# Kernel optimization log

Measured on AMD Instinct MI355X. Metric: run time of the kernel, lower is better.

Reference implementation:

```python
import jax, jax.numpy as jnp
import numpy as np

N, E, F, H, O, B = 100000, 1200000, 64, 1024, 1, 256


def _gcn_conv(x, W, b, src, dst, ew, num_nodes):
    # PyG GCNConv: out_i = sum_{(s->i)} d_i^{-1/2} w_e d_s^{-1/2} (x_s W) + b
    deg = jax.ops.segment_sum(ew, dst, num_segments=num_nodes)
    dinv = jnp.where(deg > 0, jax.lax.rsqrt(jnp.maximum(deg, 1e-12)), 0.0)
    norm = dinv[src] * ew * dinv[dst]          # [E]
    h = x @ W                                   # [N, out]
    msg = h[src] * norm[:, None]                # gather + scale
    return jax.ops.segment_sum(msg, dst, num_segments=num_nodes) + b


def setup_inputs() -> dict:
    key = jax.random.key(0)
    ks = jax.random.split(key, 12)
    def lin(k, fan_in, fan_out):
        s = 1.0 / np.sqrt(fan_in)
        kw, kb = jax.random.split(k)
        return (jax.random.uniform(kw, (fan_in, fan_out), jnp.float32, -s, s),
                jax.random.uniform(kb, (fan_out,), jnp.float32, -s, s))
    W1, b1 = lin(ks[0], F, F)
    W2, b2 = lin(ks[1], F, 2 * F)
    W3, b3 = lin(ks[2], 2 * F, 4 * F)
    Wf1, bf1 = lin(ks[3], 5 * F, H)
    Wf2, bf2 = lin(ks[4], H, O)
    feature = jax.random.normal(ks[5], (N, F), jnp.float32)
    edge_index = jax.random.randint(ks[6], (2, E), 0, N, jnp.int32)
    weight = jax.random.uniform(ks[7], (E,), jnp.float32)
    protein_batch = jnp.sort(jax.random.randint(ks[8], (N,), 0, B, jnp.int32))
    return {"feature": feature, "edge_index": edge_index, "weight": weight,
            "protein_batch": protein_batch,
            "W1": W1, "b1": b1, "W2": W2, "b2": b2, "W3": W3, "b3": b3,
            "Wf1": Wf1, "bf1": bf1, "Wf2": Wf2, "bf2": bf2}


def reference(feature, edge_index, weight, protein_batch,
              W1, b1, W2, b2, W3, b3, Wf1, bf1, Wf2, bf2):
    num_nodes = feature.shape[0]
    # add self-loops with weight 1 (PyG default)
    loop = jnp.arange(num_nodes, dtype=edge_index.dtype)
    src = jnp.concatenate([edge_index[0], loop])
    dst = jnp.concatenate([edge_index[1], loop])
    ew = jnp.concatenate([weight, jnp.ones((num_nodes,), weight.dtype)])

    x = jax.nn.relu(_gcn_conv(feature, W1, b1, src, dst, ew, num_nodes))
    x = jax.nn.relu(_gcn_conv(x, W2, b2, src, dst, ew, num_nodes))
    x = jax.nn.relu(_gcn_conv(x, W3, b3, src, dst, ew, num_nodes))
    x = jnp.concatenate([x, feature], axis=1)   # [N, 5F]

    # global_mean_pool over graph ids
    sums = jax.ops.segment_sum(x, protein_batch, num_segments=B)
    cnts = jax.ops.segment_sum(jnp.ones((num_nodes,), x.dtype), protein_batch, num_segments=B)
    gc = sums / jnp.maximum(cnts, 1.0)[:, None]

    gc = jax.nn.relu(gc @ Wf1 + bf1)            # dropout is identity in eval
    return gc @ Wf2 + bf2
```

## Files before the change

kernel.cpp:

```cpp
#include <hip/hip_runtime.h>
#include <cstdio>
#include <cstdint>

typedef _Float16 f16x8 __attribute__((ext_vector_type(8)));
typedef float f32x4 __attribute__((ext_vector_type(4)));

__device__ inline unsigned short f2bf(float f) {
  unsigned u = __float_as_uint(f);
  u += 0x7fffu + ((u >> 16) & 1u);
  return (unsigned short)(u >> 16);
}
__device__ inline float bf2f(unsigned short h) {
  return __uint_as_float(((unsigned)h) << 16);
}
__device__ inline unsigned short f2h(float f) {
  union { _Float16 h; unsigned short u; } cv;
  cv.h = (_Float16)f;
  return cv.u;
}


__global__ __launch_bounds__(256)
void k_prep(unsigned long long* __restrict__ packed, double* __restrict__ psum,
            float* __restrict__ gcnt,
            const float* __restrict__ feature, ushort* __restrict__ featb,
            const float* __restrict__ W1, ushort* __restrict__ w1h,
            const float* __restrict__ W2, ushort* __restrict__ w2h,
            const float* __restrict__ W3, ushort* __restrict__ w3h,
            int N, int BC, int Bn, int NF, int F, int D2, int D3,
            int nA, int nB, int nC) {
  int b = blockIdx.x;
  int t = threadIdx.x;
  if (b < nA) {
    int i = b * 256 + t;
    if (i < N) packed[i] = 0ull;
  } else if (b < nA + nB) {
    int i = (b - nA) * 256 + t;
    if (i < BC) psum[i] = 0.0;
    if (i < Bn) gcnt[i] = 0.f;
  } else if (b < nA + nB + nC) {
    int base = ((b - nA - nB) * 256 + t) * 4;
    if (base < NF) {
      float4 v = *reinterpret_cast<const float4*>(feature + base);
      ushort4 h;
      h.x = f2bf(v.x); h.y = f2bf(v.y); h.z = f2bf(v.z); h.w = f2bf(v.w);
      *reinterpret_cast<ushort4*>(featb + base) = h;
    }
  } else {
    int idx = (b - nA - nB - nC) * 256 + t;
    int s1 = F * F, s2 = s1 + F * D2, s3 = s2 + D2 * D3;
    if (idx < s1) {
      int k = idx / F, n = idx - k * F;
      w1h[(size_t)n * F + k] = f2h(W1[idx]);
    } else if (idx < s2) {
      int i2 = idx - s1; int k = i2 / D2, n = i2 - k * D2;
      w2h[(size_t)n * F + k] = f2h(W2[i2]);
    } else if (idx < s3) {
      int i3 = idx - s2; int k = i3 / D3, n = i3 - k * D3;
      w3h[(size_t)n * D2 + k] = f2h(W3[i3]);
    }
  }
}


__global__ __launch_bounds__(256)
void k_count_pack(const int* __restrict__ dst, const float* __restrict__ ew,
                  unsigned long long* __restrict__ packed,
                  int* __restrict__ rank, int E) {
  const int b0 = blockIdx.x * 1024 + threadIdx.x;
  int d[4]; float w[4]; unsigned long long old[4];
#pragma unroll
  for (int j = 0; j < 4; j++) {
    int e = b0 + 256 * j;
    if (e < E) { d[j] = dst[e]; w[j] = ew[e]; }
  }
#pragma unroll
  for (int j = 0; j < 4; j++) {
    int e = b0 + 256 * j;
    if (e < E) {
      unsigned long long q = (unsigned long long)(w[j] * 1073741824.0f + 0.5f);
      old[j] = atomicAdd(&packed[d[j]], (1ull << 40) | q);
    }
  }
#pragma unroll
  for (int j = 0; j < 4; j++) {
    int e = b0 + 256 * j;
    if (e < E) rank[e] = (int)(old[j] >> 40);
  }
}

__global__ __launch_bounds__(256)
void k_scan1(const unsigned long long* __restrict__ packed, int* __restrict__ rs,
             int* __restrict__ bsum, float* __restrict__ dinv,
             float* __restrict__ sn, int N) {
  __shared__ int sh[256];
  const int t = threadIdx.x;
  const int base = blockIdx.x * 1024;
  int v[4]; int s = 0;
#pragma unroll
  for (int j = 0; j < 4; j++) {
    int idx = base + t * 4 + j;
    if (idx < N) {
      unsigned long long p = packed[idx];
      v[j] = (int)(p >> 40);
      double deg = 1.0 + (double)(p & 0xFFFFFFFFFFull) * (1.0 / 1073741824.0);
      float r = (float)(1.0 / sqrt(deg));
      dinv[idx] = r;
      sn[idx] = r * r;
    } else v[j] = 0;
    s += v[j];
  }
  sh[t] = s;
  __syncthreads();
  for (int off = 1; off < 256; off <<= 1) {
    int x = (t >= off) ? sh[t - off] : 0;
    __syncthreads();
    sh[t] += x;
    __syncthreads();
  }
  int run = sh[t] - s;
#pragma unroll
  for (int j = 0; j < 4; j++) {
    int idx = base + t * 4 + j;
    if (idx < N) rs[idx] = run;
    run += v[j];
  }
  if (t == 255) bsum[blockIdx.x] = sh[255];
}

__global__ __launch_bounds__(256)
void k_scan23(int* __restrict__ rs, const int* __restrict__ bsum, int N, int E) {
  __shared__ int spre;
  const int chunk = blockIdx.x >> 2;
  if (threadIdx.x == 0) {
    int pre = 0;
    for (int t = 0; t < chunk; t++) pre += bsum[t];
    spre = pre;
  }
  __syncthreads();
  int i = blockIdx.x * 256 + threadIdx.x;
  if (i < N) rs[i] += spre;
  if (i == 0) rs[N] = E;
}

__global__ void k_csr_fill(const int* __restrict__ src, const int* __restrict__ dst,
                           const float* __restrict__ ew, const float* __restrict__ dinv,
                           const int* __restrict__ rs, const int* __restrict__ rank,
                           int2* __restrict__ epack, int E) {
  int e = blockIdx.x * blockDim.x + threadIdx.x;
  if (e >= E) return;
  int d = dst[e], s = src[e];
  int pos = rs[d] + rank[e];
  float w = dinv[s] * ew[e] * dinv[d];
  epack[pos] = make_int2(s, __float_as_int(w));
}


__device__ inline void bf8_fma(const int4 v, float w, float* acc) {
  acc[0] = fmaf(__uint_as_float((unsigned)v.x << 16), w, acc[0]);
  acc[1] = fmaf(__uint_as_float((unsigned)v.x & 0xffff0000u), w, acc[1]);
  acc[2] = fmaf(__uint_as_float((unsigned)v.y << 16), w, acc[2]);
  acc[3] = fmaf(__uint_as_float((unsigned)v.y & 0xffff0000u), w, acc[3]);
  acc[4] = fmaf(__uint_as_float((unsigned)v.z << 16), w, acc[4]);
  acc[5] = fmaf(__uint_as_float((unsigned)v.z & 0xffff0000u), w, acc[5]);
  acc[6] = fmaf(__uint_as_float((unsigned)v.w << 16), w, acc[6]);
  acc[7] = fmaf(__uint_as_float((unsigned)v.w & 0xffff0000u), w, acc[7]);
}

template<int LOG2L>
__global__ __launch_bounds__(256)
void k_aggregate_b(const ushort* __restrict__ Xb, const int* __restrict__ rs,
                   const int2* __restrict__ epack, const float* __restrict__ sn,
                   ushort* __restrict__ AH, int N) {
  const int t = blockIdx.x * blockDim.x + threadIdx.x;
  const int row = t >> LOG2L;
  if (row >= N) return;
  const int L = 1 << LOG2L;
  const int D = L << 3;
  const int c = (t & (L - 1)) << 3;

  float acc[8];
  {
    int4 v = *reinterpret_cast<const int4*>(Xb + (size_t)row * D + c);
    float s = sn[row];
    acc[0] = s * __uint_as_float((unsigned)v.x << 16);
    acc[1] = s * __uint_as_float((unsigned)v.x & 0xffff0000u);
    acc[2] = s * __uint_as_float((unsigned)v.y << 16);
    acc[3] = s * __uint_as_float((unsigned)v.y & 0xffff0000u);
    acc[4] = s * __uint_as_float((unsigned)v.z << 16);
    acc[5] = s * __uint_as_float((unsigned)v.z & 0xffff0000u);
    acc[6] = s * __uint_as_float((unsigned)v.w << 16);
    acc[7] = s * __uint_as_float((unsigned)v.w & 0xffff0000u);
  }
  const int p0 = rs[row], pe = rs[row + 1];
  int i = p0;
  if ((i & 1) && i < pe) {
    int2 e = epack[i];
    int4 v = *reinterpret_cast<const int4*>(Xb + (size_t)e.x * D + c);
    bf8_fma(v, __int_as_float(e.y), acc);
    i++;
  }
  for (; i + 2 <= pe; i += 2) {
    int4 e2 = *reinterpret_cast<const int4*>(&epack[i]);
    int4 v0 = *reinterpret_cast<const int4*>(Xb + (size_t)e2.x * D + c);
    int4 v1 = *reinterpret_cast<const int4*>(Xb + (size_t)e2.z * D + c);
    bf8_fma(v0, __int_as_float(e2.y), acc);
    bf8_fma(v1, __int_as_float(e2.w), acc);
  }
  if (i < pe) {
    int2 e = epack[i];
    int4 v = *reinterpret_cast<const int4*>(Xb + (size_t)e.x * D + c);
    bf8_fma(v, __int_as_float(e.y), acc);
  }
  ushort h[8];
#pragma unroll
  for (int j = 0; j < 8; j++) h[j] = f2h(acc[j]);
  size_t o = (size_t)row * D + c;
  *reinterpret_cast<ushort4*>(AH + o)     = make_ushort4(h[0], h[1], h[2], h[3]);
  *reinterpret_cast<ushort4*>(AH + o + 4) = make_ushort4(h[4], h[5], h[6], h[7]);
}


template<int KT, int NT>
__global__ __launch_bounds__(256)
void k_gemm_mfma(const ushort* __restrict__ Ah, const ushort* __restrict__ Bh,
                 const float* __restrict__ bias, ushort* __restrict__ Y,
                 int N, int D) {
  constexpr int PK = 72;
  __shared__ __align__(16) ushort sAh[128 * PK];
  __shared__ __align__(16) ushort sBh[NT * PK];
  const int t = threadIdx.x;
  const int wave = t >> 6, lane = t & 63;
  const int quad = lane >> 4, l16 = lane & 15;
  const int m0 = blockIdx.y * 128;
  const int n0 = blockIdx.x * NT;

  f32x4 acc[2][NT / 16];
#pragma unroll
  for (int mi = 0; mi < 2; mi++)
#pragma unroll
    for (int ni = 0; ni < NT / 16; ni++) acc[mi][ni] = (f32x4){0.f, 0.f, 0.f, 0.f};

  for (int k0 = 0; k0 < KT; k0 += 64) {
    if (k0) __syncthreads();
#pragma unroll
    for (int it = 0; it < 4; it++) {
      int c = t + 256 * it;
      int row = c >> 3, kc = (c & 7) << 3;
      int gr = m0 + row; if (gr >= N) gr = N - 1;
      *reinterpret_cast<int4*>(&sAh[row * PK + kc]) =
          *reinterpret_cast<const int4*>(Ah + (size_t)gr * KT + k0 + kc);
    }
#pragma unroll
    for (int it = 0; it < NT / 32; it++) {
      int c = t + 256 * it;
      int row = c >> 3, kc = (c & 7) << 3;
      *reinterpret_cast<int4*>(&sBh[row * PK + kc]) =
          *reinterpret_cast<const int4*>(Bh + (size_t)(n0 + row) * KT + k0 + kc);
    }
    __syncthreads();
#pragma unroll
    for (int ks = 0; ks < 2; ks++) {
      const int kk = ks * 32 + quad * 8;
      f16x8 aH[2];
#pragma unroll
      for (int mi = 0; mi < 2; mi++) {
        int r = wave * 32 + mi * 16 + l16;
        aH[mi] = *reinterpret_cast<const f16x8*>(&sAh[r * PK + kk]);
      }
#pragma unroll
      for (int ni = 0; ni < NT / 16; ni++) {
        int r = ni * 16 + l16;
        f16x8 bH = *reinterpret_cast<const f16x8*>(&sBh[r * PK + kk]);
#pragma unroll
        for (int mi = 0; mi < 2; mi++)
          acc[mi][ni] = __builtin_amdgcn_mfma_f32_16x16x32_f16(aH[mi], bH, acc[mi][ni], 0, 0, 0);
      }
    }
  }
#pragma unroll
  for (int mi = 0; mi < 2; mi++) {
    int rb = m0 + wave * 32 + mi * 16 + quad * 4;
#pragma unroll
    for (int ni = 0; ni < NT / 16; ni++) {
      int col = n0 + ni * 16 + l16;
      float bv = bias[col];
#pragma unroll
      for (int r = 0; r < 4; r++) {
        int row = rb + r;
        if (row < N)
          Y[(size_t)row * D + col] = f2bf(fmaxf(acc[mi][ni][r] + bv, 0.f));
      }
    }
  }
}


__global__ void k_pool(const ushort* __restrict__ X3b, const float* __restrict__ feat,
                       const int* __restrict__ pb, double* __restrict__ psum,
                       int N, int D3, int F) {
  const int c = threadIdx.x;
  const int C = D3 + F;
  int i0 = blockIdx.x * 64;
  if (i0 >= N) return;
  int iend = i0 + 64; if (iend > N) iend = N;
  double acc = 0.0;
  int cur = pb[i0];
  for (int i = i0; i < iend; i++) {
    int b = pb[i];
    if (b != cur) {
      atomicAdd(&psum[(size_t)cur * C + c], acc);
      acc = 0.0; cur = b;
    }
    float v;
    if (c < D3) v = bf2f(X3b[(size_t)i * D3 + c]);
    else        v = feat[(size_t)i * F + (c - D3)];
    acc += (double)v;
  }
  atomicAdd(&psum[(size_t)cur * C + c], acc);
}

__global__ void k_count(const int* __restrict__ pb, float* __restrict__ cnt, int N) {
  int tchunk = blockIdx.x * blockDim.x + threadIdx.x;
  int i0 = tchunk * 64;
  if (i0 >= N) return;
  int iend = i0 + 64; if (iend > N) iend = N;
  float cacc = 0.f; int cur = pb[i0];
  for (int i = i0; i < iend; i++) {
    int b = pb[i];
    if (b != cur) { atomicAdd(&cnt[cur], cacc); cacc = 0.f; cur = b; }
    cacc += 1.f;
  }
  atomicAdd(&cnt[cur], cacc);
}


__global__ __launch_bounds__(256)
void k_fc1(const double* __restrict__ psum, const float* __restrict__ cnt,
           const float* __restrict__ Wf1, const float* __restrict__ bf1,
           float* __restrict__ hidden, int C, int Hh) {
  const int b = blockIdx.y;
  __shared__ float gcs[384];
  float invc = 1.f / fmaxf(cnt[b], 1.f);
  for (int c = threadIdx.x; c < C; c += 256)
    gcs[c] = (float)psum[(size_t)b * C + c] * invc;
  __syncthreads();
  const int j = blockIdx.x * 256 + threadIdx.x;
  if (j >= Hh) return;
  const float* w = Wf1 + j;
  float a0 = 0.f, a1 = 0.f, a2 = 0.f, a3 = 0.f;
  int c = 0;
  for (; c + 4 <= C; c += 4) {
    a0 = fmaf(gcs[c + 0], w[(size_t)(c + 0) * Hh], a0);
    a1 = fmaf(gcs[c + 1], w[(size_t)(c + 1) * Hh], a1);
    a2 = fmaf(gcs[c + 2], w[(size_t)(c + 2) * Hh], a2);
    a3 = fmaf(gcs[c + 3], w[(size_t)(c + 3) * Hh], a3);
  }
  for (; c < C; c++) a0 = fmaf(gcs[c], w[(size_t)c * Hh], a0);
  float r = ((a0 + a1) + (a2 + a3)) + bf1[j];
  hidden[(size_t)b * Hh + j] = fmaxf(r, 0.f);
}

__global__ void k_fc2(const float* __restrict__ hidden, const float* __restrict__ Wf2,
                      const float* __restrict__ bf2, float* __restrict__ out, int Hh) {
  int b = blockIdx.x;
  int lane = threadIdx.x;
  double s = 0.0;
  for (int j = lane; j < Hh; j += 64) s += (double)hidden[(size_t)b * Hh + j] * (double)Wf2[j];
#pragma unroll
  for (int off = 32; off > 0; off >>= 1) s += __shfl_down(s, off);
  if (lane == 0) out[b] = (float)s + bf2[0];
}


extern "C" void kernel_launch(void* const* d_in, const int* in_sizes, int n_in,
                              void* d_out, int out_size, void* d_ws, size_t ws_size,
                              hipStream_t stream) {
  const float* feature = (const float*)d_in[0];
  const int*   eidx    = (const int*)  d_in[1];
  const float* weight  = (const float*)d_in[2];
  const int*   pb      = (const int*)  d_in[3];
  const float* W1  = (const float*)d_in[4];
  const float* b1  = (const float*)d_in[5];
  const float* W2  = (const float*)d_in[6];
  const float* b2  = (const float*)d_in[7];
  const float* W3  = (const float*)d_in[8];
  const float* b3  = (const float*)d_in[9];
  const float* Wf1 = (const float*)d_in[10];
  const float* bf1 = (const float*)d_in[11];
  const float* Wf2 = (const float*)d_in[12];
  const float* bf2 = (const float*)d_in[13];

  const int F  = in_sizes[5];
  const int D2 = in_sizes[7];
  const int D3 = in_sizes[9];
  const int Hh = in_sizes[11];
  const int N  = in_sizes[0] / F;
  const int E  = in_sizes[1] / 2;
  const int B  = out_size;
  const int C  = D3 + F;

  const int* srcp = eidx;
  const int* dstp = eidx + E;
  const int nscan = (N + 1023) / 1024;

  auto al = [](size_t x) { return (x + 255) & ~(size_t)255; };
  size_t off = 0;
  auto alloc = [&](size_t bytes) { size_t o = off; off += al(bytes); return o; };
  size_t o_pack  = alloc((size_t)N * 8);
  size_t o_dinv  = alloc((size_t)N * 4);
  size_t o_sn    = alloc((size_t)N * 4);
  size_t o_rs    = alloc((size_t)(N + 1) * 4);
  size_t o_rank  = alloc((size_t)E * 4);
  size_t o_bsum  = alloc((size_t)nscan * 4);
  size_t o_epack = alloc((size_t)E * 8);
  size_t o_featb = alloc((size_t)N * F  * 2);
  size_t o_x1b   = alloc((size_t)N * F  * 2);
  size_t o_x2b   = alloc((size_t)N * D2 * 2);
  size_t o_x3b   = alloc((size_t)N * D3 * 2);
  size_t o_aggh  = alloc((size_t)N * D2 * 2);
  size_t o_w1h   = alloc((size_t)F  * F  * 2);
  size_t o_w2h   = alloc((size_t)F  * D2 * 2);
  size_t o_w3h   = alloc((size_t)D2 * D3 * 2);
  size_t o_psum  = alloc((size_t)B * C * 8);
  size_t o_gcnt  = alloc((size_t)B * 4);
  size_t o_hid   = alloc((size_t)B * Hh * 4);
  if (off > ws_size) {
    fprintf(stderr, "kernel_launch: workspace too small: need %zu, have %zu\n", off, ws_size);
    return;
  }

  char* ws = (char*)d_ws;
  unsigned long long* packed = (unsigned long long*)(ws + o_pack);
  float*  dinv  = (float*)(ws + o_dinv);
  float*  sn    = (float*)(ws + o_sn);
  int*    rs    = (int*)  (ws + o_rs);
  int*    rank  = (int*)  (ws + o_rank);
  int*    bsum  = (int*)  (ws + o_bsum);
  int2*   epack = (int2*) (ws + o_epack);
  ushort* featb = (ushort*)(ws + o_featb);
  ushort* x1b   = (ushort*)(ws + o_x1b);
  ushort* x2b   = (ushort*)(ws + o_x2b);
  ushort* x3b   = (ushort*)(ws + o_x3b);
  ushort* aggh  = (ushort*)(ws + o_aggh);
  ushort* w1h   = (ushort*)(ws + o_w1h);
  ushort* w2h   = (ushort*)(ws + o_w2h);
  ushort* w3h   = (ushort*)(ws + o_w3h);
  double* psum  = (double*)(ws + o_psum);
  float*  gcnt  = (float*)(ws + o_gcnt);
  float*  hid   = (float*)(ws + o_hid);
  float*  out   = (float*)d_out;

  const int BC = B * C, NF = N * F;
  const int nA = (N + 255) / 256;
  const int nB = (BC + 255) / 256;
  const int nC = (NF / 4 + 255) / 256;
  const int nD = (F * F + F * D2 + D2 * D3 + 255) / 256;
  k_prep<<<nA + nB + nC + nD, 256, 0, stream>>>(
      packed, psum, gcnt, feature, featb, W1, w1h, W2, w2h, W3, w3h,
      N, BC, B, NF, F, D2, D3, nA, nB, nC);

  k_count_pack<<<(E + 1023) / 1024, 256, 0, stream>>>(dstp, weight, packed, rank, E);
  k_scan1     <<<nscan, 256, 0, stream>>>(packed, rs, bsum, dinv, sn, N);
  k_scan23    <<<(N + 255) / 256, 256, 0, stream>>>(rs, bsum, N, E);
  k_csr_fill  <<<(E + 255) / 256, 256, 0, stream>>>(srcp, dstp, weight, dinv, rs, rank, epack, E);

  const int gy = (N + 127) / 128;

  {
    int tot = N * (F / 8);
    k_aggregate_b<3><<<(tot + 255) / 256, 256, 0, stream>>>(featb, rs, epack, sn, aggh, N);
    dim3 g(1, gy);
    k_gemm_mfma<64, 64><<<g, 256, 0, stream>>>(aggh, w1h, b1, x1b, N, F);
  }
  {
    int tot = N * (F / 8);
    k_aggregate_b<3><<<(tot + 255) / 256, 256, 0, stream>>>(x1b, rs, epack, sn, aggh, N);
    dim3 g(1, gy);
    k_gemm_mfma<64, 128><<<g, 256, 0, stream>>>(aggh, w2h, b2, x2b, N, D2);
  }
  {
    int tot = N * (D2 / 8);
    k_aggregate_b<4><<<(tot + 255) / 256, 256, 0, stream>>>(x2b, rs, epack, sn, aggh, N);
    dim3 g(2, gy);
    k_gemm_mfma<128, 128><<<g, 256, 0, stream>>>(aggh, w3h, b3, x3b, N, D3);
  }

  k_count<<<((N + 63) / 64 + 255) / 256, 256, 0, stream>>>(pb, gcnt, N);
  k_pool <<<(N + 63) / 64, C, 0, stream>>>(x3b, feature, pb, psum, N, D3, F);
  {
    dim3 g((Hh + 255) / 256, B);
    k_fc1<<<g, 256, 0, stream>>>(psum, gcnt, Wf1, bf1, hid, C, Hh);
  }
  k_fc2  <<<B, 64, 0, stream>>>(hid, Wf2, bf2, out, Hh);
}
```

Before: 457.9 us.

## Build CSR via two-level bucket sort instead of global 64-bit atomics

Replaces the per-node global 64-bit atomic counting and packing with a bucketed approach: a per-block histogram over 256-node bins, a scan over the bin/block table, a scatter into bin-sorted order, and per-bin shared-memory atomics that compute per-node counts, weight sums and ranks. The CSR fill then reads edges in bin order, so its writes are more local. The intent is to move contended, randomly addressed global atomics into LDS and improve locality. It also folds the graph-count kernel into the pool kernel. In exchange it adds several launches and extra intermediate buffers, and float LDS atomics make the degree sums order-dependent.

```diff
diff --git a/kernel.cpp b/kernel.cpp
--- a/kernel.cpp
+++ b/kernel.cpp
@@ -21,25 +21,21 @@
 
 
 __global__ __launch_bounds__(256)
-void k_prep(unsigned long long* __restrict__ packed, double* __restrict__ psum,
-            float* __restrict__ gcnt,
+void k_prep(double* __restrict__ psum, float* __restrict__ gcnt,
             const float* __restrict__ feature, ushort* __restrict__ featb,
             const float* __restrict__ W1, ushort* __restrict__ w1h,
             const float* __restrict__ W2, ushort* __restrict__ w2h,
             const float* __restrict__ W3, ushort* __restrict__ w3h,
-            int N, int BC, int Bn, int NF, int F, int D2, int D3,
-            int nA, int nB, int nC) {
+            int BC, int Bn, int NF, int F, int D2, int D3,
+            int nB, int nC) {
   int b = blockIdx.x;
   int t = threadIdx.x;
-  if (b < nA) {
+  if (b < nB) {
     int i = b * 256 + t;
-    if (i < N) packed[i] = 0ull;
-  } else if (b < nA + nB) {
-    int i = (b - nA) * 256 + t;
     if (i < BC) psum[i] = 0.0;
     if (i < Bn) gcnt[i] = 0.f;
-  } else if (b < nA + nB + nC) {
-    int base = ((b - nA - nB) * 256 + t) * 4;
+  } else if (b < nB + nC) {
+    int base = ((b - nB) * 256 + t) * 4;
     if (base < NF) {
       float4 v = *reinterpret_cast<const float4*>(feature + base);
       ushort4 h;
@@ -47,7 +43,7 @@
       *reinterpret_cast<ushort4*>(featb + base) = h;
     }
   } else {
-    int idx = (b - nA - nB - nC) * 256 + t;
+    int idx = (b - nB - nC) * 256 + t;
     int s1 = F * F, s2 = s1 + F * D2, s3 = s2 + D2 * D3;
     if (idx < s1) {
       int k = idx / F, n = idx - k * F;
@@ -64,35 +60,25 @@
 
 
 __global__ __launch_bounds__(256)
-void k_count_pack(const int* __restrict__ dst, const float* __restrict__ ew,
-                  unsigned long long* __restrict__ packed,
-                  int* __restrict__ rank, int E) {
-  const int b0 = blockIdx.x * 1024 + threadIdx.x;
-  int d[4]; float w[4]; unsigned long long old[4];
+void k_bhist(const int* __restrict__ dst, int* __restrict__ H,
+             int NB, int E) {
+  __shared__ int hist[512];
+  const int t = threadIdx.x;
+  for (int i = t; i < NB; i += 256) hist[i] = 0;
+  __syncthreads();
+  const int base = blockIdx.x * 1024 + t;
 #pragma unroll
   for (int j = 0; j < 4; j++) {
-    int e = b0 + 256 * j;
-    if (e < E) { d[j] = dst[e]; w[j] = ew[e]; }
-  }
-#pragma unroll
-  for (int j = 0; j < 4; j++) {
-    int e = b0 + 256 * j;
-    if (e < E) {
-      unsigned long long q = (unsigned long long)(w[j] * 1073741824.0f + 0.5f);
-      old[j] = atomicAdd(&packed[d[j]], (1ull << 40) | q);
-    }
-  }
-#pragma unroll
-  for (int j = 0; j < 4; j++) {
-    int e = b0 + 256 * j;
-    if (e < E) rank[e] = (int)(old[j] >> 40);
-  }
-}
-
-__global__ __launch_bounds__(256)
-void k_scan1(const unsigned long long* __restrict__ packed, int* __restrict__ rs,
-             int* __restrict__ bsum, float* __restrict__ dinv,
-             float* __restrict__ sn, int N) {
+    int e = base + 256 * j;
+    if (e < E) atomicAdd(&hist[dst[e] >> 8], 1);
+  }
+  __syncthreads();
+  for (int i = t; i < NB; i += 256) H[(size_t)blockIdx.x * NB + i] = hist[i];
+}
+
+__global__ __launch_bounds__(256)
+void k_bscan1(const int* __restrict__ H, int* __restrict__ S,
+              int* __restrict__ bsum, int NB, int NBLK, int T) {
   __shared__ int sh[256];
   const int t = threadIdx.x;
   const int base = blockIdx.x * 1024;
@@ -100,10 +86,108 @@
 #pragma unroll
   for (int j = 0; j < 4; j++) {
     int idx = base + t * 4 + j;
+    if (idx < T) {
+      int bin = idx / NBLK, bi = idx - bin * NBLK;
+      v[j] = H[(size_t)bi * NB + bin];
+    } else v[j] = 0;
+    s += v[j];
+  }
+  sh[t] = s;
+  __syncthreads();
+  for (int off = 1; off < 256; off <<= 1) {
+    int x = (t >= off) ? sh[t - off] : 0;
+    __syncthreads();
+    sh[t] += x;
+    __syncthreads();
+  }
+  int run = sh[t] - s;
+#pragma unroll
+  for (int j = 0; j < 4; j++) {
+    int idx = base + t * 4 + j;
+    if (idx < T) S[idx] = run;
+    run += v[j];
+  }
+  if (t == 255) bsum[blockIdx.x] = sh[255];
+}
+
+__global__ __launch_bounds__(256)
+void k_bscan23(int* __restrict__ S, const int* __restrict__ bsum, int T) {
+  __shared__ int spre;
+  const int chunk = blockIdx.x >> 2;
+  if (threadIdx.x == 0) {
+    int pre = 0;
+    for (int t = 0; t < chunk; t++) pre += bsum[t];
+    spre = pre;
+  }
+  __syncthreads();
+  int i = blockIdx.x * 256 + threadIdx.x;
+  if (i < T) S[i] += spre;
+}
+
+__global__ __launch_bounds__(256)
+void k_bscatter(const int* __restrict__ src, const int* __restrict__ dst,
+                const float* __restrict__ ew, const int* __restrict__ S,
+                int* __restrict__ sdst, int2* __restrict__ ssw,
+                int NB, int NBLK, int E) {
+  __shared__ int cnt[512];
+  __shared__ int sbase[512];
+  const int t = threadIdx.x, bi = blockIdx.x;
+  for (int i = t; i < NB; i += 256) {
+    cnt[i] = 0;
+    sbase[i] = S[(size_t)i * NBLK + bi];
+  }
+  __syncthreads();
+  const int base = bi * 1024 + t;
+#pragma unroll
+  for (int j = 0; j < 4; j++) {
+    int e = base + 256 * j;
+    if (e < E) {
+      int d = dst[e];
+      int bin = d >> 8;
+      int r = atomicAdd(&cnt[bin], 1);
+      int pos = sbase[bin] + r;
+      sdst[pos] = d;
+      ssw[pos] = make_int2(src[e], __float_as_int(ew[e]));
+    }
+  }
+}
+
+__global__ __launch_bounds__(256)
+void k_bproc(const int* __restrict__ sdst, const int2* __restrict__ ssw,
+             const int* __restrict__ S, int* __restrict__ rank2,
+             int* __restrict__ cntN, float* __restrict__ wsumN,
+             int NB, int NBLK, int N, int E) {
+  __shared__ int cnt[256];
+  __shared__ float wsm[256];
+  const int t = threadIdx.x, bin = blockIdx.x;
+  cnt[t] = 0; wsm[t] = 0.f;
+  __syncthreads();
+  const int start = S[(size_t)bin * NBLK];
+  const int end = (bin + 1 < NB) ? S[(size_t)(bin + 1) * NBLK] : E;
+  for (int p = start + t; p < end; p += 256) {
+    int ld = sdst[p] & 255;
+    rank2[p] = atomicAdd(&cnt[ld], 1);
+    atomicAdd(&wsm[ld], __int_as_float(ssw[p].y));
+  }
+  __syncthreads();
+  int n = bin * 256 + t;
+  if (n < N) { cntN[n] = cnt[t]; wsumN[n] = wsm[t]; }
+}
+
+__global__ __launch_bounds__(256)
+void k_scan1(const int* __restrict__ cntN, const float* __restrict__ wsumN,
+             int* __restrict__ rs, int* __restrict__ bsum,
+             float* __restrict__ dinv, float* __restrict__ sn, int N) {
+  __shared__ int sh[256];
+  const int t = threadIdx.x;
+  const int base = blockIdx.x * 1024;
+  int v[4]; int s = 0;
+#pragma unroll
+  for (int j = 0; j < 4; j++) {
+    int idx = base + t * 4 + j;
     if (idx < N) {
-      unsigned long long p = packed[idx];
-      v[j] = (int)(p >> 40);
-      double deg = 1.0 + (double)(p & 0xFFFFFFFFFFull) * (1.0 / 1073741824.0);
+      v[j] = cntN[idx];
+      double deg = 1.0 + (double)wsumN[idx];
       float r = (float)(1.0 / sqrt(deg));
       dinv[idx] = r;
       sn[idx] = r * r;
@@ -143,16 +227,16 @@
   if (i == 0) rs[N] = E;
 }
 
-__global__ void k_csr_fill(const int* __restrict__ src, const int* __restrict__ dst,
-                           const float* __restrict__ ew, const float* __restrict__ dinv,
-                           const int* __restrict__ rs, const int* __restrict__ rank,
-                           int2* __restrict__ epack, int E) {
-  int e = blockIdx.x * blockDim.x + threadIdx.x;
-  if (e >= E) return;
-  int d = dst[e], s = src[e];
-  int pos = rs[d] + rank[e];
-  float w = dinv[s] * ew[e] * dinv[d];
-  epack[pos] = make_int2(s, __float_as_int(w));
+__global__ void k_csr_fill2(const int* __restrict__ sdst, const int2* __restrict__ ssw,
+                            const int* __restrict__ rank2, const int* __restrict__ rs,
+                            const float* __restrict__ dinv,
+                            int2* __restrict__ epack, int E) {
+  int p = blockIdx.x * blockDim.x + threadIdx.x;
+  if (p >= E) return;
+  int d = sdst[p];
+  int2 sw = ssw[p];
+  float w = dinv[sw.x] * __int_as_float(sw.y) * dinv[d];
+  epack[rs[d] + rank2[p]] = make_int2(sw.x, __float_as_int(w));
 }
 
 
@@ -298,40 +382,30 @@
 
 __global__ void k_pool(const ushort* __restrict__ X3b, const float* __restrict__ feat,
                        const int* __restrict__ pb, double* __restrict__ psum,
-                       int N, int D3, int F) {
+                       float* __restrict__ gcnt, int N, int D3, int F) {
   const int c = threadIdx.x;
   const int C = D3 + F;
   int i0 = blockIdx.x * 64;
   if (i0 >= N) return;
   int iend = i0 + 64; if (iend > N) iend = N;
   double acc = 0.0;
+  float cacc = 0.f;
   int cur = pb[i0];
   for (int i = i0; i < iend; i++) {
     int b = pb[i];
     if (b != cur) {
       atomicAdd(&psum[(size_t)cur * C + c], acc);
-      acc = 0.0; cur = b;
+      if (c == 0) atomicAdd(&gcnt[cur], cacc);
+      acc = 0.0; cacc = 0.f; cur = b;
     }
     float v;
     if (c < D3) v = bf2f(X3b[(size_t)i * D3 + c]);
     else        v = feat[(size_t)i * F + (c - D3)];
     acc += (double)v;
+    cacc += 1.f;
   }
   atomicAdd(&psum[(size_t)cur * C + c], acc);
-}
-
-__global__ void k_count(const int* __restrict__ pb, float* __restrict__ cnt, int N) {
-  int tchunk = blockIdx.x * blockDim.x + threadIdx.x;
-  int i0 = tchunk * 64;
-  if (i0 >= N) return;
-  int iend = i0 + 64; if (iend > N) iend = N;
-  float cacc = 0.f; int cur = pb[i0];
-  for (int i = i0; i < iend; i++) {
-    int b = pb[i];
-    if (b != cur) { atomicAdd(&cnt[cur], cacc); cacc = 0.f; cur = b; }
-    cacc += 1.f;
-  }
-  atomicAdd(&cnt[cur], cacc);
+  if (c == 0) atomicAdd(&gcnt[cur], cacc);
 }
 
 
@@ -402,16 +476,27 @@
 
   const int* srcp = eidx;
   const int* dstp = eidx + E;
-  const int nscan = (N + 1023) / 1024;
+
+  const int NB   = (N + 255) / 256;
+  const int NBLK = (E + 1023) / 1024;
+  const int T    = NB * NBLK;
+  const int nscanb = (T + 1023) / 1024;
+  const int nscan  = (N + 1023) / 1024;
 
   auto al = [](size_t x) { return (x + 255) & ~(size_t)255; };
   size_t off = 0;
   auto alloc = [&](size_t bytes) { size_t o = off; off += al(bytes); return o; };
-  size_t o_pack  = alloc((size_t)N * 8);
+  size_t o_H     = alloc((size_t)T * 4);
+  size_t o_S     = alloc((size_t)T * 4);
+  size_t o_bsb   = alloc((size_t)nscanb * 4);
+  size_t o_sdst  = alloc((size_t)E * 4);
+  size_t o_ssw   = alloc((size_t)E * 8);
+  size_t o_rank2 = alloc((size_t)E * 4);
+  size_t o_cntN  = alloc((size_t)N * 4);
+  size_t o_wsumN = alloc((size_t)N * 4);
   size_t o_dinv  = alloc((size_t)N * 4);
   size_t o_sn    = alloc((size_t)N * 4);
   size_t o_rs    = alloc((size_t)(N + 1) * 4);
-  size_t o_rank  = alloc((size_t)E * 4);
   size_t o_bsum  = alloc((size_t)nscan * 4);
   size_t o_epack = alloc((size_t)E * 8);
   size_t o_featb = alloc((size_t)N * F  * 2);
@@ -431,11 +516,17 @@
   }
 
   char* ws = (char*)d_ws;
-  unsigned long long* packed = (unsigned long long*)(ws + o_pack);
+  int*    H     = (int*)  (ws + o_H);
+  int*    S     = (int*)  (ws + o_S);
+  int*    bsb   = (int*)  (ws + o_bsb);
+  int*    sdst  = (int*)  (ws + o_sdst);
+  int2*   ssw   = (int2*) (ws + o_ssw);
+  int*    rank2 = (int*)  (ws + o_rank2);
+  int*    cntN  = (int*)  (ws + o_cntN);
+  float*  wsumN = (float*)(ws + o_wsumN);
   float*  dinv  = (float*)(ws + o_dinv);
   float*  sn    = (float*)(ws + o_sn);
   int*    rs    = (int*)  (ws + o_rs);
-  int*    rank  = (int*)  (ws + o_rank);
   int*    bsum  = (int*)  (ws + o_bsum);
   int2*   epack = (int2*) (ws + o_epack);
   ushort* featb = (ushort*)(ws + o_featb);
@@ -452,18 +543,21 @@
   float*  out   = (float*)d_out;
 
   const int BC = B * C, NF = N * F;
-  const int nA = (N + 255) / 256;
   const int nB = (BC + 255) / 256;
   const int nC = (NF / 4 + 255) / 256;
   const int nD = (F * F + F * D2 + D2 * D3 + 255) / 256;
-  k_prep<<<nA + nB + nC + nD, 256, 0, stream>>>(
-      packed, psum, gcnt, feature, featb, W1, w1h, W2, w2h, W3, w3h,
-      N, BC, B, NF, F, D2, D3, nA, nB, nC);
-
-  k_count_pack<<<(E + 1023) / 1024, 256, 0, stream>>>(dstp, weight, packed, rank, E);
-  k_scan1     <<<nscan, 256, 0, stream>>>(packed, rs, bsum, dinv, sn, N);
-  k_scan23    <<<(N + 255) / 256, 256, 0, stream>>>(rs, bsum, N, E);
-  k_csr_fill  <<<(E + 255) / 256, 256, 0, stream>>>(srcp, dstp, weight, dinv, rs, rank, epack, E);
+  k_prep<<<nB + nC + nD, 256, 0, stream>>>(
+      psum, gcnt, feature, featb, W1, w1h, W2, w2h, W3, w3h,
+      BC, B, NF, F, D2, D3, nB, nC);
+
+  k_bhist   <<<NBLK, 256, 0, stream>>>(dstp, H, NB, E);
+  k_bscan1  <<<nscanb, 256, 0, stream>>>(H, S, bsb, NB, NBLK, T);
+  k_bscan23 <<<(T + 255) / 256, 256, 0, stream>>>(S, bsb, T);
+  k_bscatter<<<NBLK, 256, 0, stream>>>(srcp, dstp, weight, S, sdst, ssw, NB, NBLK, E);
+  k_bproc   <<<NB, 256, 0, stream>>>(sdst, ssw, S, rank2, cntN, wsumN, NB, NBLK, N, E);
+  k_scan1   <<<nscan, 256, 0, stream>>>(cntN, wsumN, rs, bsum, dinv, sn, N);
+  k_scan23  <<<(N + 255) / 256, 256, 0, stream>>>(rs, bsum, N, E);
+  k_csr_fill2<<<(E + 255) / 256, 256, 0, stream>>>(sdst, ssw, rank2, rs, dinv, epack, E);
 
   const int gy = (N + 127) / 128;
 
@@ -486,8 +580,7 @@
     k_gemm_mfma<128, 128><<<g, 256, 0, stream>>>(aggh, w3h, b3, x3b, N, D3);
   }
 
-  k_count<<<((N + 63) / 64 + 255) / 256, 256, 0, stream>>>(pb, gcnt, N);
-  k_pool <<<(N + 63) / 64, C, 0, stream>>>(x3b, feature, pb, psum, N, D3, F);
+  k_pool <<<(N + 63) / 64, C, 0, stream>>>(x3b, feature, pb, psum, gcnt, N, D3, F);
   {
     dim3 g((Hh + 255) / 256, B);
     k_fc1<<<g, 256, 0, stream>>>(psum, gcnt, Wf1, bf1, hid, C, Hh);
```

Result: faster. 442.0 us (-3.5%).
